# Optimization experiments

Measured on AMD Instinct MI355X. Metric: run time of the kernel, lower is better.

## Reference

```python
import jax, jax.numpy as jnp
import numpy as np

N_EMBD = 1024
N_HEAD = 16
HEAD_SIZE = N_EMBD // N_HEAD
D_FF = 4 * N_EMBD
B, T = 4, 2048
EPS = 1e-5


def _layernorm(x, w, b):
    mu = jnp.mean(x, axis=-1, keepdims=True)
    var = jnp.mean(jnp.square(x - mu), axis=-1, keepdims=True)
    return (x - mu) * jax.lax.rsqrt(var + EPS) * w + b


def setup_inputs() -> dict:
    key = jax.random.key(0)
    ks = jax.random.split(key, 12)
    s = 0.02
    x = jax.random.normal(ks[0], (B, T, N_EMBD), dtype=jnp.float32)
    # right-padded prefix mask: lengths in [T//2, T] -> no all-masked causal rows
    lengths = jax.random.randint(ks[1], (B,), T // 2, T + 1)
    key_padding_mask = jnp.arange(T)[None, :] < lengths[:, None]  # [B,T] bool, True=keep
    wq = jax.random.normal(ks[2], (N_EMBD, N_HEAD, HEAD_SIZE), dtype=jnp.float32) * s
    wk = jax.random.normal(ks[3], (N_EMBD, N_HEAD, HEAD_SIZE), dtype=jnp.float32) * s
    wv = jax.random.normal(ks[4], (N_EMBD, N_HEAD, HEAD_SIZE), dtype=jnp.float32) * s
    proj_w = jax.random.normal(ks[5], (N_EMBD, N_EMBD), dtype=jnp.float32) * s
    proj_b = jnp.zeros((N_EMBD,), dtype=jnp.float32)
    ff_w1 = jax.random.normal(ks[6], (N_EMBD, D_FF), dtype=jnp.float32) * s
    ff_b1 = jnp.zeros((D_FF,), dtype=jnp.float32)
    ff_w2 = jax.random.normal(ks[7], (D_FF, N_EMBD), dtype=jnp.float32) * s
    ff_b2 = jnp.zeros((N_EMBD,), dtype=jnp.float32)
    ln1_w = jnp.ones((N_EMBD,), dtype=jnp.float32)
    ln1_b = jnp.zeros((N_EMBD,), dtype=jnp.float32)
    ln2_w = jnp.ones((N_EMBD,), dtype=jnp.float32)
    ln2_b = jnp.zeros((N_EMBD,), dtype=jnp.float32)
    return dict(x=x, key_padding_mask=key_padding_mask, wq=wq, wk=wk, wv=wv,
                proj_w=proj_w, proj_b=proj_b, ff_w1=ff_w1, ff_b1=ff_b1,
                ff_w2=ff_w2, ff_b2=ff_b2, ln1_w=ln1_w, ln1_b=ln1_b,
                ln2_w=ln2_w, ln2_b=ln2_b)


def reference(x, key_padding_mask, wq, wk, wv, proj_w, proj_b,
              ff_w1, ff_b1, ff_w2, ff_b2, ln1_w, ln1_b, ln2_w, ln2_b):
    Bn, Tn, C = x.shape
    m = key_padding_mask.astype(x.dtype)  # [B,T]
    # --- attention sublayer ---
    h = _layernorm(x, ln1_w, ln1_b) * m[..., None]
    q = jnp.einsum('btc,chd->bhtd', h, wq)
    k = jnp.einsum('btc,chd->bhtd', h, wk)
    v = jnp.einsum('btc,chd->bhtd', h, wv)
    # NOTE: original scales by full embed dim C**-0.5, not head_size
    scores = jnp.einsum('bhtd,bhsd->bhts', q, k) * (C ** -0.5)
    causal = jnp.tril(jnp.ones((Tn, Tn), dtype=bool))
    mask = causal[None, None, :, :] & key_padding_mask[:, None, None, :]
    scores = jnp.where(mask, scores, -jnp.inf)
    wei = jax.nn.softmax(scores, axis=-1)
    out = jnp.einsum('bhts,bhsd->bthd', wei, v).reshape(Bn, Tn, C)
    x = x + out @ proj_w + proj_b
    # --- feedforward sublayer ---
    h2 = _layernorm(x, ln2_w, ln2_b) * m[..., None]
    ff = jax.nn.relu(h2 @ ff_w1 + ff_b1) @ ff_w2 + ff_b2
    x = (x + ff) * m[..., None]
    return x
```

## Files before the change

### kernel.cpp

```cpp
#include <hip/hip_runtime.h>
#include <math.h>

typedef float f32x4 __attribute__((ext_vector_type(4)));
typedef float f4 __attribute__((ext_vector_type(4)));
typedef __bf16 bf16x8 __attribute__((ext_vector_type(8)));
typedef __bf16 bf16x4 __attribute__((ext_vector_type(4)));

#define GLOBAL_AS __attribute__((address_space(1)))
#define LDS_AS __attribute__((address_space(3)))

__global__ __launch_bounds__(256) void mask_canon(const unsigned char* __restrict__ raw,
                                                  float* __restrict__ msk, int n) {
    int i = blockIdx.x * 256 + threadIdx.x;
    if (i >= n) return;
    unsigned int w0 = *(const unsigned int*)raw;
    float v;
    if (w0 == 0x01010101u)       v = raw[i] ? 1.f : 0.f;
    else if (w0 == 0x3f800000u)  v = ((const float*)raw)[i];
    else                         v = ((const int*)raw)[i] ? 1.f : 0.f;
    msk[i] = v;
}

__global__ __launch_bounds__(256) void lens_kernel(const float* __restrict__ msk,
                                                   float* __restrict__ lens) {
    int b = blockIdx.x, tid = threadIdx.x;
    float s = 0.f;
    for (int i = tid; i < 2048; i += 256) s += msk[b * 2048 + i];
#pragma unroll
    for (int off = 1; off < 64; off <<= 1) s += __shfl_xor(s, off);
    __shared__ float red[4];
    int wave = tid >> 6, lane = tid & 63;
    if (lane == 0) red[wave] = s;
    __syncthreads();
    if (tid == 0) lens[b] = red[0] + red[1] + red[2] + red[3];
}

__global__ __launch_bounds__(256) void tcvt(const float* __restrict__ src,
                                            __bf16* __restrict__ dst, int K, int N) {
    __shared__ float tile[32][33];
    int n0 = blockIdx.x * 32, k0 = blockIdx.y * 32;
    int tx = threadIdx.x & 31, ty = threadIdx.x >> 5;
#pragma unroll
    for (int i = 0; i < 4; ++i)
        tile[ty + 8 * i][tx] = src[(long)(k0 + ty + 8 * i) * N + n0 + tx];
    __syncthreads();
#pragma unroll
    for (int i = 0; i < 4; ++i)
        dst[(long)(n0 + ty + 8 * i) * K + k0 + tx] = (__bf16)tile[tx][ty + 8 * i];
}

__global__ __launch_bounds__(256) void ln_kernel(const float* __restrict__ x,
                                                 const float* __restrict__ w,
                                                 const float* __restrict__ bsc,
                                                 const float* __restrict__ msk,
                                                 __bf16* __restrict__ out) {
    long row = blockIdx.x;
    int tid = threadIdx.x;
    f4 xv = *(const f4*)(x + row * 1024 + tid * 4);
    float s = xv[0] + xv[1] + xv[2] + xv[3];
    float sq = xv[0] * xv[0] + xv[1] * xv[1] + xv[2] * xv[2] + xv[3] * xv[3];
#pragma unroll
    for (int off = 1; off < 64; off <<= 1) {
        s += __shfl_xor(s, off);
        sq += __shfl_xor(sq, off);
    }
    __shared__ float red[2][4];
    int wave = tid >> 6, lane = tid & 63;
    if (lane == 0) { red[0][wave] = s; red[1][wave] = sq; }
    __syncthreads();
    s = red[0][0] + red[0][1] + red[0][2] + red[0][3];
    sq = red[1][0] + red[1][1] + red[1][2] + red[1][3];
    float mu = s * (1.0f / 1024.0f);
    float var = sq * (1.0f / 1024.0f) - mu * mu;
    float rs = rsqrtf(var + 1e-5f);
    float mv = msk[row];
    f4 wv = *(const f4*)(w + tid * 4);
    f4 bv = *(const f4*)(bsc + tid * 4);
    bf16x4 ov;
#pragma unroll
    for (int j = 0; j < 4; ++j)
        ov[j] = (__bf16)(((xv[j] - mu) * rs * wv[j] + bv[j]) * mv);
    *(bf16x4*)(out + row * 1024 + tid * 4) = ov;
}

#define BARRIER   __asm__ volatile("s_barrier" ::: "memory")
#define LGKM0     __asm__ volatile("s_waitcnt lgkmcnt(0)" ::: "memory")
#define PRIO1     __builtin_amdgcn_s_setprio(1)
#define PRIO0     __builtin_amdgcn_s_setprio(0)

template <int EP>
__global__ __launch_bounds__(512, 2) void gemm_bt8(const __bf16* __restrict__ A,
                                                   const __bf16* __restrict__ B,
                                                   int K, int N, void* __restrict__ Cout,
                                                   const float* __restrict__ bias) {
    __shared__ __bf16 As[2][2][128 * 64];
    __shared__ __bf16 Bs[2][2][128 * 64];
    int tid = threadIdx.x;
    int wave = tid >> 6, lane = tid & 63;
    int l15 = lane & 15, quad = lane >> 4;
    int r8 = l15 & 7;
    int wm = wave >> 2, wn = wave & 3;
    long rowBase = (long)blockIdx.x * 256;
    long colBase = (long)blockIdx.y * 256;
    const __bf16* Ab = A + rowBase * K;
    const __bf16* Bb = B + colBase * K;
    int srow = lane >> 3;
    int scol = ((lane & 7) ^ srow) * 8;
    f32x4 acc[8][4] = {};

#define STGA(d_, h_, kt_)                                                                   \
    do {                                                                                    \
        _Pragma("unroll") for (int j = 0; j < 2; ++j) {                                     \
            const __bf16* g_ = Ab + (long)((h_) * 128 + wave * 16 + j * 8 + srow) * K +     \
                               (kt_) + scol;                                                \
            __builtin_amdgcn_global_load_lds(                                               \
                (const GLOBAL_AS void*)g_,                                                  \
                (LDS_AS void*)((char*)&As[d_][h_][0] + wave * 2048 + j * 1024), 16, 0, 0);  \
        }                                                                                   \
    } while (0)
#define STGB(d_, h_, kt_)                                                                   \
    do {                                                                                    \
        _Pragma("unroll") for (int j = 0; j < 2; ++j) {                                     \
            const __bf16* g_ = Bb + (long)((h_) * 128 + wave * 16 + j * 8 + srow) * K +     \
                               (kt_) + scol;                                                \
            __builtin_amdgcn_global_load_lds(                                               \
                (const GLOBAL_AS void*)g_,                                                  \
                (LDS_AS void*)((char*)&Bs[d_][h_][0] + wave * 2048 + j * 1024), 16, 0, 0);  \
        }                                                                                   \
    } while (0)
#define RDA(mh)                                                                      \
    do {                                                                             \
        _Pragma("unroll") for (int mi = 0; mi < 4; ++mi) {                           \
            int row_ = (mh) * 64 + mi * 16 + l15;                                    \
            af[mi][0] = *(const bf16x8*)(Ac + row_ * 64 + ((quad ^ r8) << 3));       \
            af[mi][1] = *(const bf16x8*)(Ac + row_ * 64 + (((4 + quad) ^ r8) << 3)); \
        }                                                                            \
    } while (0)
#define RDB(h)                                                                           \
    do {                                                                                 \
        _Pragma("unroll") for (int ni = 0; ni < 2; ++ni) {                               \
            int row_ = (wn & 1) * 64 + ((h) * 2 + ni) * 16 + l15;                        \
            bfr[h][ni][0] = *(const bf16x8*)(Bc + row_ * 64 + ((quad ^ r8) << 3));       \
            bfr[h][ni][1] = *(const bf16x8*)(Bc + row_ * 64 + (((4 + quad) ^ r8) << 3)); \
        }                                                                                \
    } while (0)
#define MM(mh, nh)                                                                          \
    do {                                                                                    \
        PRIO1;                                                                              \
        _Pragma("unroll") for (int mi = 0; mi < 4; ++mi) {                                  \
            _Pragma("unroll") for (int ni = 0; ni < 2; ++ni) {                              \
                acc[(mh) * 4 + mi][(nh) * 2 + ni] = __builtin_amdgcn_mfma_f32_16x16x32_bf16(\
                    af[mi][0], bfr[nh][ni][0], acc[(mh) * 4 + mi][(nh) * 2 + ni], 0, 0, 0); \
                acc[(mh) * 4 + mi][(nh) * 2 + ni] = __builtin_amdgcn_mfma_f32_16x16x32_bf16(\
                    af[mi][1], bfr[nh][ni][1], acc[(mh) * 4 + mi][(nh) * 2 + ni], 0, 0, 0); \
            }                                                                               \
        }                                                                                   \
        PRIO0;                                                                              \
    } while (0)

    const int NT = K >> 6;
    STGA(0, 0, 0); STGA(0, 1, 0); STGB(0, 0, 0); STGB(0, 1, 0);
    STGB(1, 0, 64); STGB(1, 1, 64);
    __asm__ volatile("s_waitcnt vmcnt(4)" ::: "memory");
    BARRIER;

    bf16x8 af[4][2], bfr[2][2][2];
    int kt = 0;
    for (int t = 0; t < NT; ++t, kt += 64) {
        int d = t & 1;
        const __bf16* Ac = &As[d][wm][0];
        const __bf16* Bc = &Bs[d][wn >> 1][0];
        const bool haveA1 = (t + 1 < NT), haveB2 = (t + 2 < NT);
        RDA(0); RDB(0);
        if (haveA1) STGA(d ^ 1, 0, kt + 64);
        BARRIER; LGKM0;
        MM(0, 0);
        BARRIER;
        RDB(1);
        if (haveA1) STGA(d ^ 1, 1, kt + 64);
        BARRIER; LGKM0;
        MM(0, 1);
        BARRIER;
        RDA(1);
        if (haveB2) STGB(d, 0, kt + 128);
        BARRIER; LGKM0;
        MM(1, 1);
        BARRIER;
        if (haveB2) {
            STGB(d, 1, kt + 128);
            __asm__ volatile("s_waitcnt vmcnt(4)" ::: "memory");
        } else {
            __asm__ volatile("s_waitcnt vmcnt(0)" ::: "memory");
        }
        BARRIER;
        MM(1, 0);
        BARRIER;
    }
#undef STGA
#undef STGB
#undef RDA
#undef RDB
#undef MM

#pragma unroll
    for (int mi = 0; mi < 8; ++mi) {
#pragma unroll
        for (int r = 0; r < 4; ++r) {
            long gr = rowBase + wm * 128 + mi * 16 + quad * 4 + r;
#pragma unroll
            for (int ni = 0; ni < 4; ++ni) {
                long gc = colBase + wn * 64 + ni * 16 + l15;
                float v = acc[mi][ni][r];
                if constexpr (EP == 0) {
                    ((__bf16*)Cout)[gr * N + gc] = (__bf16)v;
                } else {
                    v += bias[gc];
                    v = v > 0.f ? v : 0.f;
                    ((__bf16*)Cout)[gr * N + gc] = (__bf16)v;
                }
            }
        }
    }
}

template <int EP>
__global__ __launch_bounds__(512, 2) void gemm_bt8n(const __bf16* __restrict__ A,
                                                    const __bf16* __restrict__ B,
                                                    int K, int N, void* __restrict__ Cout,
                                                    const float* __restrict__ bias,
                                                    const float* __restrict__ resid,
                                                    const float* __restrict__ mskp) {
    __shared__ __bf16 As2[2][2][128 * 64];
    __shared__ __bf16 Bs2[2][2][64 * 64];
    int tid = threadIdx.x;
    int wave = tid >> 6, lane = tid & 63;
    int l15 = lane & 15, quad = lane >> 4;
    int r8 = l15 & 7;
    int wm = wave >> 1, wn = wave & 1;
    long rowBase = (long)blockIdx.x * 256;
    long colBase = (long)blockIdx.y * 128;
    const __bf16* Ab = A + rowBase * K;
    const __bf16* Bb = B + colBase * K;
    int srow = lane >> 3;
    int scol = ((lane & 7) ^ srow) * 8;
    f32x4 acc[4][4] = {};

#define NSTGA(d_, h_, kt_)                                                                  \
    do {                                                                                    \
        _Pragma("unroll") for (int j = 0; j < 2; ++j) {                                     \
            const __bf16* g_ = Ab + (long)((h_) * 128 + wave * 16 + j * 8 + srow) * K +     \
                               (kt_) + scol;                                                \
            __builtin_amdgcn_global_load_lds(                                               \
                (const GLOBAL_AS void*)g_,                                                  \
                (LDS_AS void*)((char*)&As2[d_][h_][0] + wave * 2048 + j * 1024), 16, 0, 0); \
        }                                                                                   \
    } while (0)
#define NSTGB(d_, h_, kt_)                                                                  \
    do {                                                                                    \
        const __bf16* g_ = Bb + (long)((h_) * 64 + wave * 8 + srow) * K + (kt_) + scol;     \
        __builtin_amdgcn_global_load_lds(                                                   \
            (const GLOBAL_AS void*)g_,                                                      \
            (LDS_AS void*)((char*)&Bs2[d_][h_][0] + wave * 1024), 16, 0, 0);                \
    } while (0)
#define NRA(H)                                                                           \
    do {                                                                                 \
        _Pragma("unroll") for (int mi = 0; mi < 2; ++mi) {                               \
            int row_ = (wm & 1) * 64 + ((H) * 2 + mi) * 16 + l15;                        \
            afr[H][mi][0] = *(const bf16x8*)(Ac + row_ * 64 + ((quad ^ r8) << 3));       \
            afr[H][mi][1] = *(const bf16x8*)(Ac + row_ * 64 + (((4 + quad) ^ r8) << 3)); \
        }                                                                                \
    } while (0)
#define NRB(H)                                                                            \
    do {                                                                                  \
        _Pragma("unroll") for (int ni = 0; ni < 2; ++ni) {                                \
            int row_ = ((H) * 2 + ni) * 16 + l15;                                         \
            bfr2[H][ni][0] = *(const bf16x8*)(Bc + row_ * 64 + ((quad ^ r8) << 3));       \
            bfr2[H][ni][1] = *(const bf16x8*)(Bc + row_ * 64 + (((4 + quad) ^ r8) << 3)); \
        }                                                                                 \
    } while (0)
#define NMM(AH, BH)                                                                          \
    do {                                                                                     \
        PRIO1;                                                                               \
        _Pragma("unroll") for (int mi = 0; mi < 2; ++mi) {                                   \
            _Pragma("unroll") for (int ni = 0; ni < 2; ++ni) {                               \
                acc[(AH) * 2 + mi][(BH) * 2 + ni] = __builtin_amdgcn_mfma_f32_16x16x32_bf16( \
                    afr[AH][mi][0], bfr2[BH][ni][0], acc[(AH) * 2 + mi][(BH) * 2 + ni], 0,   \
                    0, 0);                                                                   \
                acc[(AH) * 2 + mi][(BH) * 2 + ni] = __builtin_amdgcn_mfma_f32_16x16x32_bf16( \
                    afr[AH][mi][1], bfr2[BH][ni][1], acc[(AH) * 2 + mi][(BH) * 2 + ni], 0,   \
                    0, 0);                                                                   \
            }                                                                                \
        }                                                                                    \
        PRIO0;                                                                               \
    } while (0)

    const int NT = K >> 6;
    NSTGA(0, 0, 0); NSTGA(0, 1, 0); NSTGB(0, 0, 0); NSTGB(0, 1, 0);
    NSTGB(1, 0, 64); NSTGB(1, 1, 64);
    __asm__ volatile("s_waitcnt vmcnt(2)" ::: "memory");
    BARRIER;

    bf16x8 afr[2][2][2], bfr2[2][2][2];
    int kt = 0;
    for (int t = 0; t < NT; ++t, kt += 64) {
        int d = t & 1;
        const __bf16* Ac = &As2[d][wm >> 1][0];
        const __bf16* Bc = &Bs2[d][wn][0];
        const bool haveA1 = (t + 1 < NT), haveB2 = (t + 2 < NT);
        NRA(0); NRB(0);
        if (haveA1) NSTGA(d ^ 1, 0, kt + 64);
        BARRIER; LGKM0;
        NMM(0, 0);
        BARRIER;
        NRB(1);
        if (haveA1) NSTGA(d ^ 1, 1, kt + 64);
        BARRIER; LGKM0;
        NMM(0, 1);
        BARRIER;
        NRA(1);
        if (haveB2) NSTGB(d, 0, kt + 128);
        BARRIER; LGKM0;
        NMM(1, 1);
        BARRIER;
        if (haveB2) {
            NSTGB(d, 1, kt + 128);
            __asm__ volatile("s_waitcnt vmcnt(2)" ::: "memory");
        } else {
            __asm__ volatile("s_waitcnt vmcnt(0)" ::: "memory");
        }
        BARRIER;
        NMM(1, 0);
        BARRIER;
    }
#undef NSTGA
#undef NSTGB
#undef NRA
#undef NRB
#undef NMM

#pragma unroll
    for (int mi = 0; mi < 4; ++mi) {
#pragma unroll
        for (int r = 0; r < 4; ++r) {
            long gr = rowBase + wm * 64 + mi * 16 + quad * 4 + r;
#pragma unroll
            for (int ni = 0; ni < 4; ++ni) {
                long gc = colBase + wn * 64 + ni * 16 + l15;
                float v = acc[mi][ni][r];
                if constexpr (EP == 2) {
                    v += bias[gc] + resid[gr * N + gc];
                    ((float*)Cout)[gr * N + gc] = v;
                } else {
                    v = (v + bias[gc] + resid[gr * N + gc]) * mskp[gr];
                    ((float*)Cout)[gr * N + gc] = v;
                }
            }
        }
    }
}

#define SWIZ(row, d) ((row) * 64 + ((((d) >> 3) ^ ((row) & 7)) << 3) + ((d) & 7))
__global__ __launch_bounds__(256, 3) void attn_kernel(const __bf16* __restrict__ qkv,
                                                      const float* __restrict__ lens,
                                                      __bf16* __restrict__ att) {
    const int T = 2048, C3 = 3072;
    int bh = blockIdx.x;
    int qt = 15 - blockIdx.y;
    int h = bh & 15, b = bh >> 4;
    int tid = threadIdx.x;
    int wave = tid >> 6, lane = tid & 63, l15 = lane & 15, quad = lane >> 4;

    __shared__ __bf16 Kl[64 * 64];
    __shared__ __bf16 Vt[64 * 64];
    __shared__ __bf16 Pl[4][32 * 64];

    long rowB = (long)b * T;
    const __bf16* kbase = qkv + rowB * C3 + 1024 + h * 64;
    const __bf16* vbase = qkv + rowB * C3 + 2048 + h * 64;
    const float scale2 = (1.0f / 32.0f) * 1.44269504088896f;

    int krow = tid >> 2, kd = (tid & 3) * 16;
    int vk = (tid & 15) * 4, vd = (tid >> 4) * 4;
    int vc8 = vk >> 3, vk7 = vk & 7;

    bf16x8 ones;
#pragma unroll
    for (int j = 0; j < 8; ++j) ones[j] = (__bf16)1.0f;

    __bf16* pw = &Pl[wave][0];
    int r8 = l15 & 7;

    int qbase = qt * 128;
    int wq0 = qbase + wave * 32;

    bf16x8 qf[2][2];
#pragma unroll
    for (int g = 0; g < 2; ++g) {
        const __bf16* qptr = qkv + (rowB + wq0 + g * 16 + l15) * C3 + h * 64;
        qf[g][0] = *(const bf16x8*)(qptr + quad * 8);
        qf[g][1] = *(const bf16x8*)(qptr + 32 + quad * 8);
    }

    f32x4 o0[4] = {}, o1[4] = {};
    f32x4 lacc0 = {}, lacc1 = {};
    int nchunk = 2 * qt + 2;
    float len = lens[b];

    bf16x8 kpre0, kpre1;
    bf16x4 vpre[4];
    {
        const __bf16* kg = kbase + (long)krow * C3 + kd;
        kpre0 = *(const bf16x8*)kg;
        kpre1 = *(const bf16x8*)(kg + 8);
#pragma unroll
        for (int j = 0; j < 4; ++j)
            vpre[j] = *(const bf16x4*)(vbase + (long)(vk + j) * C3 + vd);
    }

    for (int c = 0; c < nchunk; ++c) {
        int k0 = c * 64;
        __asm__ volatile("s_barrier" ::: "memory");
        *(bf16x8*)(&Kl[SWIZ(krow, kd)]) = kpre0;
        *(bf16x8*)(&Kl[SWIZ(krow, kd + 8)]) = kpre1;
#pragma unroll
        for (int dd = 0; dd < 4; ++dd) {
            bf16x4 w = {vpre[0][dd], vpre[1][dd], vpre[2][dd], vpre[3][dd]};
            int d = vd + dd;
            *(bf16x4*)(&Vt[d * 64 + ((vc8 ^ (d & 7)) << 3) + vk7]) = w;
        }
        if (c + 1 < nchunk) {
            int k1 = k0 + 64;
            const __bf16* kg = kbase + (long)(k1 + krow) * C3 + kd;
            kpre0 = *(const bf16x8*)kg;
            kpre1 = *(const bf16x8*)(kg + 8);
#pragma unroll
            for (int j = 0; j < 4; ++j)
                vpre[j] = *(const bf16x4*)(vbase + (long)(k1 + vk + j) * C3 + vd);
        }
        __asm__ volatile("s_waitcnt lgkmcnt(0)\n\ts_barrier" ::: "memory");

        if (k0 <= wq0 + 31) {
            f32x4 s0[4] = {}, s1[4] = {};
#pragma unroll
            for (int n = 0; n < 4; ++n) {
                int row = n * 16 + l15;
                bf16x8 kb0 = *(const bf16x8*)(&Kl[row * 64 + ((quad ^ r8) << 3)]);
                bf16x8 kb1 = *(const bf16x8*)(&Kl[row * 64 + (((4 + quad) ^ r8) << 3)]);
                s0[n] = __builtin_amdgcn_mfma_f32_16x16x32_bf16(kb0, qf[0][0], s0[n], 0, 0, 0);
                s0[n] = __builtin_amdgcn_mfma_f32_16x16x32_bf16(kb1, qf[0][1], s0[n], 0, 0, 0);
                s1[n] = __builtin_amdgcn_mfma_f32_16x16x32_bf16(kb0, qf[1][0], s1[n], 0, 0, 0);
                s1[n] = __builtin_amdgcn_mfma_f32_16x16x32_bf16(kb1, qf[1][1], s1[n], 0, 0, 0);
            }

            bool needC = (k0 + 63 > wq0);
#pragma unroll
            for (int n = 0; n < 4; ++n) {
                int c8 = n * 2 + (quad >> 1);
                int sub = (quad & 1) * 4;
                bf16x4 w0, w1;
                if (!needC) {
#pragma unroll
                    for (int r = 0; r < 4; ++r) {
                        w0[r] = (__bf16)exp2f(s0[n][r] * scale2);
                        w1[r] = (__bf16)exp2f(s1[n][r] * scale2);
                    }
                } else {
                    int kg = k0 + n * 16 + quad * 4;
                    int qg0 = wq0 + l15, qg1 = wq0 + 16 + l15;
#pragma unroll
                    for (int r = 0; r < 4; ++r) {
                        w0[r] = (kg + r <= qg0) ? (__bf16)exp2f(s0[n][r] * scale2) : (__bf16)0.f;
                        w1[r] = (kg + r <= qg1) ? (__bf16)exp2f(s1[n][r] * scale2) : (__bf16)0.f;
                    }
                }
                int wbase = l15 * 64 + ((c8 ^ r8) << 3) + sub;
                *(bf16x4*)(pw + wbase) = w0;
                *(bf16x4*)(pw + 1024 + wbase) = w1;
            }
            __asm__ volatile("s_waitcnt lgkmcnt(0)" ::: "memory");

            bf16x8 pa00 = *(const bf16x8*)(pw + l15 * 64 + ((quad ^ r8) << 3));
            bf16x8 pa01 = *(const bf16x8*)(pw + l15 * 64 + (((4 + quad) ^ r8) << 3));
            bf16x8 pa10 = *(const bf16x8*)(pw + 1024 + l15 * 64 + ((quad ^ r8) << 3));
            bf16x8 pa11 = *(const bf16x8*)(pw + 1024 + l15 * 64 + (((4 + quad) ^ r8) << 3));
#pragma unroll
            for (int nd = 0; nd < 4; ++nd) {
                int row = nd * 16 + l15;
                bf16x8 vb0 = *(const bf16x8*)(&Vt[row * 64 + ((quad ^ r8) << 3)]);
                bf16x8 vb1 = *(const bf16x8*)(&Vt[row * 64 + (((4 + quad) ^ r8) << 3)]);
                o0[nd] = __builtin_amdgcn_mfma_f32_16x16x32_bf16(pa00, vb0, o0[nd], 0, 0, 0);
                o0[nd] = __builtin_amdgcn_mfma_f32_16x16x32_bf16(pa01, vb1, o0[nd], 0, 0, 0);
                o1[nd] = __builtin_amdgcn_mfma_f32_16x16x32_bf16(pa10, vb0, o1[nd], 0, 0, 0);
                o1[nd] = __builtin_amdgcn_mfma_f32_16x16x32_bf16(pa11, vb1, o1[nd], 0, 0, 0);
            }
            lacc0 = __builtin_amdgcn_mfma_f32_16x16x32_bf16(pa00, ones, lacc0, 0, 0, 0);
            lacc0 = __builtin_amdgcn_mfma_f32_16x16x32_bf16(pa01, ones, lacc0, 0, 0, 0);
            lacc1 = __builtin_amdgcn_mfma_f32_16x16x32_bf16(pa10, ones, lacc1, 0, 0, 0);
            lacc1 = __builtin_amdgcn_mfma_f32_16x16x32_bf16(pa11, ones, lacc1, 0, 0, 0);
        }
    }

#pragma unroll
    for (int r = 0; r < 4; ++r) {
        int q0g = wq0 + quad * 4 + r;
        float inv0 = 1.0f / (lacc0[r] - fmaxf(0.f, (float)(q0g + 1) - len));
        long orow0 = rowB + q0g;
        int q1g = q0g + 16;
        float inv1 = 1.0f / (lacc1[r] - fmaxf(0.f, (float)(q1g + 1) - len));
        long orow1 = rowB + q1g;
#pragma unroll
        for (int nd = 0; nd < 4; ++nd) {
            att[orow0 * 1024 + h * 64 + nd * 16 + l15] = (__bf16)(o0[nd][r] * inv0);
            att[orow1 * 1024 + h * 64 + nd * 16 + l15] = (__bf16)(o1[nd][r] * inv1);
        }
    }
}

extern "C" void kernel_launch(void* const* d_in, const int* in_sizes, int n_in,
                              void* d_out, int out_size, void* d_ws, size_t ws_size,
                              hipStream_t stream) {
    const float* x      = (const float*)d_in[0];
    const void*  kpm    = d_in[1];
    const float* wq     = (const float*)d_in[2];
    const float* wk     = (const float*)d_in[3];
    const float* wv     = (const float*)d_in[4];
    const float* proj_w = (const float*)d_in[5];
    const float* proj_b = (const float*)d_in[6];
    const float* ff_w1  = (const float*)d_in[7];
    const float* ff_b1  = (const float*)d_in[8];
    const float* ff_w2  = (const float*)d_in[9];
    const float* ff_b2  = (const float*)d_in[10];
    const float* ln1w   = (const float*)d_in[11];
    const float* ln1b   = (const float*)d_in[12];
    const float* ln2w   = (const float*)d_in[13];
    const float* ln2b   = (const float*)d_in[14];

    char* ws = (char*)d_ws;
    size_t off = 0;
    auto take = [&](size_t bytes) -> char* {
        char* p = ws + off;
        off += (bytes + 255) & ~(size_t)255;
        return p;
    };
    float*  msk    = (float*)take(8192 * 4);
    float*  lens   = (float*)take(256);
    __bf16* wqkvT  = (__bf16*)take(3072L * 1024 * 2);
    __bf16* wprojT = (__bf16*)take(1024L * 1024 * 2);
    __bf16* wff1T  = (__bf16*)take(4096L * 1024 * 2);
    __bf16* wff2T  = (__bf16*)take(4096L * 1024 * 2);
    __bf16* h1     = (__bf16*)take(8192L * 1024 * 2);
    char*   qkv_c  = take(8192L * 3072 * 2);
    __bf16* qkvb   = (__bf16*)qkv_c;
    __bf16* attb   = (__bf16*)take(8192L * 1024 * 2);
    float*  x2     = (float*)take(8192L * 1024 * 4);
    __bf16* h2     = (__bf16*)take(8192L * 1024 * 2);
    __bf16* ffh    = (__bf16*)qkv_c;

    mask_canon<<<32, 256, 0, stream>>>((const unsigned char*)kpm, msk, 8192);
    lens_kernel<<<4, 256, 0, stream>>>(msk, lens);
    tcvt<<<dim3(32, 32), 256, 0, stream>>>(wq, wqkvT, 1024, 1024);
    tcvt<<<dim3(32, 32), 256, 0, stream>>>(wk, wqkvT + 1024L * 1024, 1024, 1024);
    tcvt<<<dim3(32, 32), 256, 0, stream>>>(wv, wqkvT + 2048L * 1024, 1024, 1024);
    tcvt<<<dim3(32, 32), 256, 0, stream>>>(proj_w, wprojT, 1024, 1024);
    tcvt<<<dim3(128, 32), 256, 0, stream>>>(ff_w1, wff1T, 1024, 4096);
    tcvt<<<dim3(32, 128), 256, 0, stream>>>(ff_w2, wff2T, 4096, 1024);

    ln_kernel<<<8192, 256, 0, stream>>>(x, ln1w, ln1b, msk, h1);
    gemm_bt8<0><<<dim3(32, 12), 512, 0, stream>>>(h1, wqkvT, 1024, 3072, qkvb, nullptr);
    attn_kernel<<<dim3(64, 16), 256, 0, stream>>>(qkvb, lens, attb);
    gemm_bt8n<2><<<dim3(32, 8), 512, 0, stream>>>(attb, wprojT, 1024, 1024, x2, proj_b, x, nullptr);
    ln_kernel<<<8192, 256, 0, stream>>>(x2, ln2w, ln2b, msk, h2);
    gemm_bt8<1><<<dim3(32, 16), 512, 0, stream>>>(h2, wff1T, 1024, 4096, ffh, ff_b1);
    gemm_bt8n<3><<<dim3(32, 8), 512, 0, stream>>>(ffh, wff2T, 4096, 1024, (float*)d_out, ff_b2, x2, msk);
}
```

Before: 488.6 us.

## Split-K the FF2 GEMM with atomic accumulation onto a preinitialized output

The final FF2 GEMM (K=4096, N=1024) switches from the 256x128-tile kernel to the 256x256-tile kernel with a split-K of 2 over blockIdx.z. Partial sums are masked and added into the output with float atomics. A new preinit kernel first writes (residual + bias) * mask into the output. The aim is better tile efficiency and more parallelism for the K-heavy GEMM, at the cost of an extra full-output pass, atomic traffic, and nondeterministic summation order.

```diff
diff --git a/kernel.cpp b/kernel.cpp
--- a/kernel.cpp
+++ b/kernel.cpp
@@ -83,6 +83,21 @@
     *(bf16x4*)(out + row * 1024 + tid * 4) = ov;
 }
 
+__global__ __launch_bounds__(256) void preinit(const float* __restrict__ resid,
+                                               const float* __restrict__ bias,
+                                               const float* __restrict__ msk,
+                                               float* __restrict__ out) {
+    long i = (long)blockIdx.x * 256 + threadIdx.x;
+    long row = i >> 8;
+    f4 r = ((const f4*)resid)[i];
+    f4 b = ((const f4*)bias)[i & 255];
+    float m = msk[row];
+    f4 o;
+#pragma unroll
+    for (int j = 0; j < 4; ++j) o[j] = (r[j] + b[j]) * m;
+    ((f4*)out)[i] = o;
+}
+
 #define BARRIER   __asm__ volatile("s_barrier" ::: "memory")
 #define LGKM0     __asm__ volatile("s_waitcnt lgkmcnt(0)" ::: "memory")
 #define PRIO1     __builtin_amdgcn_s_setprio(1)
@@ -91,8 +106,10 @@
 template <int EP>
 __global__ __launch_bounds__(512, 2) void gemm_bt8(const __bf16* __restrict__ A,
                                                    const __bf16* __restrict__ B,
-                                                   int K, int N, void* __restrict__ Cout,
-                                                   const float* __restrict__ bias) {
+                                                   int K, int Ks, int N,
+                                                   void* __restrict__ Cout,
+                                                   const float* __restrict__ bias,
+                                                   const float* __restrict__ mskp) {
     __shared__ __bf16 As[2][2][128 * 64];
     __shared__ __bf16 Bs[2][2][128 * 64];
     int tid = threadIdx.x;
@@ -102,8 +119,9 @@
     int wm = wave >> 2, wn = wave & 3;
     long rowBase = (long)blockIdx.x * 256;
     long colBase = (long)blockIdx.y * 256;
-    const __bf16* Ab = A + rowBase * K;
-    const __bf16* Bb = B + colBase * K;
+    long koff = (long)blockIdx.z * K;
+    const __bf16* Ab = A + rowBase * Ks + koff;
+    const __bf16* Bb = B + colBase * Ks + koff;
     int srow = lane >> 3;
     int scol = ((lane & 7) ^ srow) * 8;
     f32x4 acc[8][4] = {};
@@ -111,7 +129,7 @@
 #define STGA(d_, h_, kt_)                                                                   \
     do {                                                                                    \
         _Pragma("unroll") for (int j = 0; j < 2; ++j) {                                     \
-            const __bf16* g_ = Ab + (long)((h_) * 128 + wave * 16 + j * 8 + srow) * K +     \
+            const __bf16* g_ = Ab + (long)((h_) * 128 + wave * 16 + j * 8 + srow) * Ks +    \
                                (kt_) + scol;                                                \
             __builtin_amdgcn_global_load_lds(                                               \
                 (const GLOBAL_AS void*)g_,                                                  \
@@ -121,7 +139,7 @@
 #define STGB(d_, h_, kt_)                                                                   \
     do {                                                                                    \
         _Pragma("unroll") for (int j = 0; j < 2; ++j) {                                     \
-            const __bf16* g_ = Bb + (long)((h_) * 128 + wave * 16 + j * 8 + srow) * K +     \
+            const __bf16* g_ = Bb + (long)((h_) * 128 + wave * 16 + j * 8 + srow) * Ks +    \
                                (kt_) + scol;                                                \
             __builtin_amdgcn_global_load_lds(                                               \
                 (const GLOBAL_AS void*)g_,                                                  \
@@ -207,16 +225,20 @@
 #pragma unroll
         for (int r = 0; r < 4; ++r) {
             long gr = rowBase + wm * 128 + mi * 16 + quad * 4 + r;
+            float m;
+            if constexpr (EP == 2) m = mskp[gr];
 #pragma unroll
             for (int ni = 0; ni < 4; ++ni) {
                 long gc = colBase + wn * 64 + ni * 16 + l15;
                 float v = acc[mi][ni][r];
                 if constexpr (EP == 0) {
                     ((__bf16*)Cout)[gr * N + gc] = (__bf16)v;
-                } else {
+                } else if constexpr (EP == 1) {
                     v += bias[gc];
                     v = v > 0.f ? v : 0.f;
                     ((__bf16*)Cout)[gr * N + gc] = (__bf16)v;
+                } else {
+                    unsafeAtomicAdd(&((float*)Cout)[gr * N + gc], v * m);
                 }
             }
         }
@@ -566,10 +588,11 @@
     tcvt<<<dim3(32, 128), 256, 0, stream>>>(ff_w2, wff2T, 4096, 1024);
 
     ln_kernel<<<8192, 256, 0, stream>>>(x, ln1w, ln1b, msk, h1);
-    gemm_bt8<0><<<dim3(32, 12), 512, 0, stream>>>(h1, wqkvT, 1024, 3072, qkvb, nullptr);
+    gemm_bt8<0><<<dim3(32, 12), 512, 0, stream>>>(h1, wqkvT, 1024, 1024, 3072, qkvb, nullptr, nullptr);
     attn_kernel<<<dim3(64, 16), 256, 0, stream>>>(qkvb, lens, attb);
     gemm_bt8n<2><<<dim3(32, 8), 512, 0, stream>>>(attb, wprojT, 1024, 1024, x2, proj_b, x, nullptr);
     ln_kernel<<<8192, 256, 0, stream>>>(x2, ln2w, ln2b, msk, h2);
-    gemm_bt8<1><<<dim3(32, 16), 512, 0, stream>>>(h2, wff1T, 1024, 4096, ffh, ff_b1);
-    gemm_bt8n<3><<<dim3(32, 8), 512, 0, stream>>>(ffh, wff2T, 4096, 1024, (float*)d_out, ff_b2, x2, msk);
-}
+    gemm_bt8<1><<<dim3(32, 16), 512, 0, stream>>>(h2, wff1T, 1024, 1024, 4096, ffh, ff_b1, nullptr);
+    preinit<<<8192, 256, 0, stream>>>(x2, ff_b2, msk, (float*)d_out);
+    gemm_bt8<2><<<dim3(32, 4, 2), 512, 0, stream>>>(ffh, wff2T, 2048, 4096, 1024, (float*)d_out, nullptr, msk);
+}
```

Result: slower. 513.3 us (+5.0%).
